# Performance work log

Measured on AMD Instinct MI355X. Metric: run time of the kernel, lower is better.

Reference implementation:

```python
import jax, jax.numpy as jnp
import numpy as np

VOCAB = 4096
N_QUESTIONS = 1024
N_YEARS = 14
D = 16
PAD_IDX = 101
LN_EPS = 1e-5


def setup_inputs() -> dict:
    key = jax.random.key(0)
    ks = jax.random.split(key, 10)
    B = 4096
    year = jax.random.randint(ks[0], (B,), 0, N_YEARS, dtype=jnp.int32)
    answer = jax.random.randint(ks[1], (B, N_QUESTIONS), 0, VOCAB, dtype=jnp.int32)
    # kaiming_normal_ on [num_emb, D]: std = sqrt(2 / fan_in) with fan_in = D
    std = np.sqrt(2.0 / D)
    ans_emb = jax.random.normal(ks[2], (VOCAB, D), dtype=jnp.float32) * std
    ans_emb = ans_emb.at[PAD_IDX].set(0.0)  # padding_idx row is zeros
    year_emb = jax.random.normal(ks[3], (N_YEARS, D), dtype=jnp.float32) * std
    q_emb = jax.random.normal(ks[4], (N_QUESTIONS, D), dtype=jnp.float32) * std
    # Linear(1, D): weight [D, 1], bias [D], default torch init U(-1, 1)
    lin_w = jax.random.uniform(ks[5], (D, 1), dtype=jnp.float32, minval=-1.0, maxval=1.0)
    lin_b = jax.random.uniform(ks[6], (D,), dtype=jnp.float32, minval=-1.0, maxval=1.0)
    ln_g = jnp.ones((D,), dtype=jnp.float32)
    ln_b = jnp.zeros((D,), dtype=jnp.float32)
    alpha = jnp.array([0.01], dtype=jnp.float32)
    beta = jnp.array([0.2], dtype=jnp.float32)
    return {"year": year, "answer": answer, "ans_emb": ans_emb, "lin_w": lin_w,
            "lin_b": lin_b, "ln_g": ln_g, "ln_b": ln_b, "year_emb": year_emb,
            "q_emb": q_emb, "alpha": alpha, "beta": beta}


def _forward(year, answer, ans_emb, lin_w, lin_b, ln_g, ln_b, year_emb, q_emb, alpha, beta):
    a_f = answer.astype(jnp.float32)                       # [B, Q]
    # continuous branch: Linear(1, D) applied to the scalar answer value
    cont = a_f[..., None] * lin_w[:, 0] + lin_b            # [B, Q, D]
    # categorical branch: embedding lookup (padding row already zeroed)
    cat = ans_emb[answer]                                  # [B, Q, D]
    is_cont = (answer <= 1)[..., None]                     # [B, Q, 1]
    placeholder = jnp.where(is_cont, cont, cat)            # branchless select
    # LayerNorm over last dim
    mu = jnp.mean(placeholder, axis=-1, keepdims=True)
    var = jnp.mean(jnp.square(placeholder - mu), axis=-1, keepdims=True)
    normed = (placeholder - mu) * jax.lax.rsqrt(var + LN_EPS) * ln_g + ln_b
    # scaled residual adds: yearly [B,1,D], question [Q,D] (dropout is eval-mode identity)
    out = normed + alpha[0] * year_emb[year][:, None, :] + beta[0] * q_emb
    return out


def reference(year, answer, ans_emb, lin_w, lin_b, ln_g, ln_b, year_emb, q_emb, alpha, beta):
    return _forward(year, answer, ans_emb, lin_w, lin_b, ln_g, ln_b, year_emb, q_emb, alpha, beta)
```

## Files before the change

kernel.cpp:

```cpp
#include <hip/hip_runtime.h>


typedef float f32x4 __attribute__((ext_vector_type(4)));

#define LN_EPS 1e-5f

template <bool QPOW2>
__global__ __launch_bounds__(256, 8) void survey_fwd(
    const int* __restrict__ year,
    const int* __restrict__ answer,
    const f32x4* __restrict__ ans_emb,
    const f32x4* __restrict__ lin_w,
    const f32x4* __restrict__ lin_b,
    const f32x4* __restrict__ ln_g,
    const f32x4* __restrict__ ln_b,
    const f32x4* __restrict__ year_emb,
    const f32x4* __restrict__ q_emb,
    const float* __restrict__ alpha,
    const float* __restrict__ beta,
    f32x4* __restrict__ out,
    int total, int Q, int qShift)
{
    const float A  = alpha[0];
    const float Bc = beta[0];

    const int sub = threadIdx.x & 3;
    const f32x4 g  = ln_g[sub];
    const f32x4 bb = ln_b[sub];

    const int stride = (int)(gridDim.x * blockDim.x);
    int i = (int)(blockIdx.x * blockDim.x + threadIdx.x);

    for (; i < total; i += stride) {
        const int row = i >> 2;
        const int a   = answer[row];

        f32x4 v = ans_emb[a * 4 + sub];

        if (a <= 1) {
            const f32x4 w  = lin_w[sub];
            const f32x4 lb = lin_b[sub];
            const float af = (float)a;
            v.x = af * w.x + lb.x;
            v.y = af * w.y + lb.y;
            v.z = af * w.z + lb.z;
            v.w = af * w.w + lb.w;
        }

        float s = v.x + v.y + v.z + v.w;
        s += __shfl_xor(s, 1);
        s += __shfl_xor(s, 2);
        const float mu = s * 0.0625f;

        const float dx = v.x - mu, dy = v.y - mu, dz = v.z - mu, dw = v.w - mu;
        float ss = dx * dx + dy * dy + dz * dz + dw * dw;
        ss += __shfl_xor(ss, 1);
        ss += __shfl_xor(ss, 2);
        const float r = rsqrtf(ss * 0.0625f + LN_EPS);

        const int b = QPOW2 ? (row >> qShift) : (row / Q);
        const int q = QPOW2 ? (row & (Q - 1)) : (row - b * Q);

        int yr;
        if (QPOW2 && qShift >= 6) {
            const int b_u = __builtin_amdgcn_readfirstlane(b);
            yr = year[b_u];
        } else {
            yr = year[b];
        }
        const f32x4 ye = year_emb[yr * 4 + sub];
        const f32x4 qe = q_emb[q * 4 + sub];

        f32x4 o;
        o.x = dx * r * g.x + bb.x + A * ye.x + Bc * qe.x;
        o.y = dy * r * g.y + bb.y + A * ye.y + Bc * qe.y;
        o.z = dz * r * g.z + bb.z + A * ye.z + Bc * qe.z;
        o.w = dw * r * g.w + bb.w + A * ye.w + Bc * qe.w;

        __builtin_nontemporal_store(o, &out[i]);
    }
}

extern "C" void kernel_launch(void* const* d_in, const int* in_sizes, int n_in,
                              void* d_out, int out_size, void* d_ws, size_t ws_size,
                              hipStream_t stream) {
    const int*   year     = (const int*)d_in[0];
    const int*   answer   = (const int*)d_in[1];
    const f32x4* ans_emb  = (const f32x4*)d_in[2];
    const f32x4* lin_w    = (const f32x4*)d_in[3];
    const f32x4* lin_b    = (const f32x4*)d_in[4];
    const f32x4* ln_g     = (const f32x4*)d_in[5];
    const f32x4* ln_b     = (const f32x4*)d_in[6];
    const f32x4* year_emb = (const f32x4*)d_in[7];
    const f32x4* q_emb    = (const f32x4*)d_in[8];
    const float* alpha    = (const float*)d_in[9];
    const float* beta     = (const float*)d_in[10];
    float*       out      = (float*)d_out;

    const int B     = in_sizes[0];
    const int nrows = in_sizes[1];
    const int Q     = nrows / B;
    const int total = nrows * 4;

    const long long total_threads = (long long)total;
    int blocks = (int)((total_threads + 255) / 256);
    if (blocks > 8192) blocks = 8192;

    const bool pow2 = (Q & (Q - 1)) == 0;
    int qShift = 0;
    while ((1 << qShift) < Q) ++qShift;

    if (pow2) {
        survey_fwd<true><<<blocks, 256, 0, stream>>>(
            year, answer, ans_emb, lin_w, lin_b, ln_g, ln_b, year_emb, q_emb,
            alpha, beta, (f32x4*)out, total, Q, qShift);
    } else {
        survey_fwd<false><<<blocks, 256, 0, stream>>>(
            year, answer, ans_emb, lin_w, lin_b, ln_g, ln_b, year_emb, q_emb,
            alpha, beta, (f32x4*)out, total, Q, qShift);
    }
}
```

Baseline: 50.77 us.

## Software-pipeline answer/embedding gathers and use DPP single-pass LayerNorm stats

```diff
diff --git a/kernel.cpp b/kernel.cpp
--- a/kernel.cpp
+++ b/kernel.cpp
@@ -4,6 +4,14 @@
 typedef float f32x4 __attribute__((ext_vector_type(4)));
 
 #define LN_EPS 1e-5f
+
+template <int CTRL>
+__device__ __forceinline__ float qperm(float x) {
+    return __int_as_float(
+        __builtin_amdgcn_mov_dpp(__float_as_int(x), CTRL, 0xF, 0xF, true));
+}
+#define XOR1(x) qperm<0xB1>(x)
+#define XOR2(x) qperm<0x4E>(x)
 
 template <bool QPOW2>
 __global__ __launch_bounds__(256, 8) void survey_fwd(
@@ -19,52 +27,55 @@
     const float* __restrict__ alpha,
     const float* __restrict__ beta,
     f32x4* __restrict__ out,
-    int total, int Q, int qShift)
+    int total, int nrows, int Q, int qShift)
 {
+    const int stride = (int)(gridDim.x * blockDim.x);
+    int i = (int)(blockIdx.x * blockDim.x + threadIdx.x);
+    if (i >= total) return;
+
     const float A  = alpha[0];
     const float Bc = beta[0];
-
-    const int sub = threadIdx.x & 3;
+    const int sub  = threadIdx.x & 3;
     const f32x4 g  = ln_g[sub];
     const f32x4 bb = ln_b[sub];
 
-    const int stride = (int)(gridDim.x * blockDim.x);
-    int i = (int)(blockIdx.x * blockDim.x + threadIdx.x);
+    const int nlast = nrows - 1;
+    int a0 = answer[i >> 2];
+    int r1 = (i + stride) >> 2;  if (r1 > nlast) r1 = nlast;
+    int a1 = answer[r1];
+    f32x4 v0 = ans_emb[a0 * 4 + sub];
 
     for (; i < total; i += stride) {
-        const int row = i >> 2;
-        const int a   = answer[row];
+        int r2 = (i + 2 * stride) >> 2;  if (r2 > nlast) r2 = nlast;
+        const int a2 = answer[r2];
+        const f32x4 v1 = ans_emb[a1 * 4 + sub];
 
-        f32x4 v = ans_emb[a * 4 + sub];
-
-        if (a <= 1) {
+        f32x4 v = v0;
+        if (a0 <= 1) {
             const f32x4 w  = lin_w[sub];
             const f32x4 lb = lin_b[sub];
-            const float af = (float)a;
+            const float af = (float)a0;
             v.x = af * w.x + lb.x;
             v.y = af * w.y + lb.y;
             v.z = af * w.z + lb.z;
             v.w = af * w.w + lb.w;
         }
 
-        float s = v.x + v.y + v.z + v.w;
-        s += __shfl_xor(s, 1);
-        s += __shfl_xor(s, 2);
-        const float mu = s * 0.0625f;
+        float s  = (v.x + v.y) + (v.z + v.w);
+        float s2 = v.x * v.x + v.y * v.y + v.z * v.z + v.w * v.w;
+        s  += XOR1(s);   s2 += XOR1(s2);
+        s  += XOR2(s);   s2 += XOR2(s2);
+        const float mu  = s * 0.0625f;
+        const float var = s2 * 0.0625f - mu * mu;
+        const float r   = rsqrtf(var + LN_EPS);
 
-        const float dx = v.x - mu, dy = v.y - mu, dz = v.z - mu, dw = v.w - mu;
-        float ss = dx * dx + dy * dy + dz * dz + dw * dw;
-        ss += __shfl_xor(ss, 1);
-        ss += __shfl_xor(ss, 2);
-        const float r = rsqrtf(ss * 0.0625f + LN_EPS);
-
+        const int row = i >> 2;
         const int b = QPOW2 ? (row >> qShift) : (row / Q);
         const int q = QPOW2 ? (row & (Q - 1)) : (row - b * Q);
 
         int yr;
         if (QPOW2 && qShift >= 6) {
-            const int b_u = __builtin_amdgcn_readfirstlane(b);
-            yr = year[b_u];
+            yr = year[__builtin_amdgcn_readfirstlane(b)];
         } else {
             yr = year[b];
         }
@@ -72,12 +83,15 @@
         const f32x4 qe = q_emb[q * 4 + sub];
 
         f32x4 o;
-        o.x = dx * r * g.x + bb.x + A * ye.x + Bc * qe.x;
-        o.y = dy * r * g.y + bb.y + A * ye.y + Bc * qe.y;
-        o.z = dz * r * g.z + bb.z + A * ye.z + Bc * qe.z;
-        o.w = dw * r * g.w + bb.w + A * ye.w + Bc * qe.w;
+        const float rgx = r * g.x, rgy = r * g.y, rgz = r * g.z, rgw = r * g.w;
+        o.x = v.x * rgx + (bb.x + A * ye.x + Bc * qe.x - mu * rgx);
+        o.y = v.y * rgy + (bb.y + A * ye.y + Bc * qe.y - mu * rgy);
+        o.z = v.z * rgz + (bb.z + A * ye.z + Bc * qe.z - mu * rgz);
+        o.w = v.w * rgw + (bb.w + A * ye.w + Bc * qe.w - mu * rgw);
 
         __builtin_nontemporal_store(o, &out[i]);
+
+        a0 = a1;  a1 = a2;  v0 = v1;
     }
 }
 
@@ -102,8 +116,7 @@
     const int Q     = nrows / B;
     const int total = nrows * 4;
 
-    const long long total_threads = (long long)total;
-    int blocks = (int)((total_threads + 255) / 256);
+    int blocks = (total + 255) / 256;
     if (blocks > 8192) blocks = 8192;
 
     const bool pow2 = (Q & (Q - 1)) == 0;
@@ -113,10 +126,10 @@
     if (pow2) {
         survey_fwd<true><<<blocks, 256, 0, stream>>>(
             year, answer, ans_emb, lin_w, lin_b, ln_g, ln_b, year_emb, q_emb,
-            alpha, beta, (f32x4*)out, total, Q, qShift);
+            alpha, beta, (f32x4*)out, total, nrows, Q, qShift);
     } else {
         survey_fwd<false><<<blocks, 256, 0, stream>>>(
             year, answer, ans_emb, lin_w, lin_b, ln_g, ln_b, year_emb, q_emb,
-            alpha, beta, (f32x4*)out, total, Q, qShift);
+            alpha, beta, (f32x4*)out, total, nrows, Q, qShift);
     }
 }
```

Result: slower. 52.53 us (+3.5%).
